# Performance work log

Hardware: AMD Instinct MI355X
Metric: run time of the kernel (lower is better)

## Reference

```python
import jax, jax.numpy as jnp
import numpy as np

N_NODES = 100000
LN_EPS = 1e-5


def setup_inputs() -> dict:
    key = jax.random.key(0)
    ks = jax.random.split(key, 5)
    d = 128
    E = 1600000
    x = jax.random.normal(ks[0], (N_NODES, d), dtype=jnp.float32)
    edge_index = jax.random.randint(ks[1], (2, E), 0, N_NODES, dtype=jnp.int64)
    # PyG Linear default init ~ kaiming-uniform-ish; simple scaled normal is fine for a reference
    W_l = jax.random.normal(ks[2], (d, d), dtype=jnp.float32) / jnp.sqrt(d).astype(jnp.float32)
    b_l = jnp.zeros((d,), dtype=jnp.float32)
    W_r = jax.random.normal(ks[3], (d, d), dtype=jnp.float32) / jnp.sqrt(d).astype(jnp.float32)
    ln_gamma = jnp.ones((d,), dtype=jnp.float32)
    ln_beta = jnp.zeros((d,), dtype=jnp.float32)
    return {"x": x, "edge_index": edge_index, "W_l": W_l, "b_l": b_l,
            "W_r": W_r, "ln_gamma": ln_gamma, "ln_beta": ln_beta}


def _sage_block(x, edge_index, W_l, b_l, W_r, ln_gamma, ln_beta):
    src, dst = edge_index[0], edge_index[1]
    # gather source features along edges, scatter-mean into destination nodes
    msg = x[src]                                            # [E, d]
    agg = jax.ops.segment_sum(msg, dst, num_segments=N_NODES)  # [N, d]
    cnt = jax.ops.segment_sum(jnp.ones_like(dst, dtype=x.dtype), dst,
                              num_segments=N_NODES)
    agg = agg / jnp.maximum(cnt, 1.0)[:, None]              # mean aggregation
    # SAGEConv: lin_l(agg) + lin_r(x); lin_l has bias, lin_r does not
    f = agg @ W_l.T + b_l + x @ W_r.T                        # [N, d]
    # GELU (exact erf form, matching torch F.gelu default)
    f = jax.nn.gelu(f, approximate=False)
    # LayerNorm over feature dim
    mu = jnp.mean(f, axis=-1, keepdims=True)
    var = jnp.var(f, axis=-1, keepdims=True)
    f = (f - mu) * jax.lax.rsqrt(var + LN_EPS) * ln_gamma + ln_beta
    # dropout is identity in eval mode; residual
    return f + x


def reference(x, edge_index, W_l, b_l, W_r, ln_gamma, ln_beta):
    return _sage_block(x, edge_index, W_l, b_l, W_r, ln_gamma, ln_beta)
```

## Files before the change

### kernel.cpp

```cpp
#include <hip/hip_runtime.h>
#include <math.h>

#define D 128
#define LN_EPS 1e-5f
#define CAP 48
#define BINW 512
#define BIN_CAP 12288
#define PA_EDGES 8192

typedef unsigned int uint;
typedef unsigned short ushort;
typedef __attribute__((ext_vector_type(8))) short short8;
typedef __attribute__((ext_vector_type(4))) float floatx4;

__device__ __forceinline__ floatx4 mfma16(short8 a, short8 b, floatx4 c) {
    return __builtin_amdgcn_mfma_f32_16x16x32_bf16(a, b, c, 0, 0, 0);
}

__device__ __forceinline__ ushort f2bf(float f) {
    uint u = __float_as_uint(f);
    u += 0x7FFFu + ((u >> 16) & 1u);
    return (ushort)(u >> 16);
}

__device__ __forceinline__ float fast_exp2(float x) {
#if __has_builtin(__builtin_amdgcn_exp2f)
    return __builtin_amdgcn_exp2f(x);
#else
    return exp2f(x);
#endif
}
__device__ __forceinline__ float fast_rcp(float x) {
#if __has_builtin(__builtin_amdgcn_rcpf)
    return __builtin_amdgcn_rcpf(x);
#else
    return 1.f / x;
#endif
}

__device__ __forceinline__ float gelu_f(float x) {
    float z = x + 0.044715f * x * x * x;
    float e = fast_exp2(fminf(2.3022082f * z, 80.f));
    return x * e * fast_rcp(e + 1.f);
}

__global__ __launch_bounds__(256) void setup_kernel(
        const float* __restrict__ x,
        const float* __restrict__ Wl, const float* __restrict__ Wr,
        ushort* __restrict__ xh, ushort* __restrict__ Wswhi,
        int* __restrict__ cursor, int* __restrict__ bin_cnt, int nbc4,
        int n_nodes, int rn) {
    const int tid = threadIdx.x;
    const int cb = blockIdx.x;
    const int g = cb & 7, cid = cb >> 3;
    const int lrow = cid * 16 + (tid >> 4);
    const int row = g * rn + lrow;
    if (row < n_nodes && lrow < rn) {
        const int base = row * D + (tid & 15) * 8;
        float4 a = *(const float4*)&x[base];
        float4 b = *(const float4*)&x[base + 4];
        union { ushort h[8]; uint4 v; } pk;
        pk.h[0] = f2bf(a.x); pk.h[1] = f2bf(a.y); pk.h[2] = f2bf(a.z); pk.h[3] = f2bf(a.w);
        pk.h[4] = f2bf(b.x); pk.h[5] = f2bf(b.y); pk.h[6] = f2bf(b.z); pk.h[7] = f2bf(b.w);
        *(uint4*)&xh[base] = pk.v;
    }
    const int t = cb * 256 + tid;
    if (t < 16)
        *(uint4*)&xh[(size_t)n_nodes * D + t * 8] = make_uint4(0u, 0u, 0u, 0u);
    if (t * 4 < n_nodes)
        *(int4*)&cursor[t * 4] = make_int4(0, 0, 0, 0);
    if (t < nbc4)
        *(int4*)&bin_cnt[t * 4] = make_int4(0, 0, 0, 0);
    if (t < 8 * 8 * 64) {
        int tt = t >> 9;
        int rem = t & 511;
        int s  = rem >> 6;
        int lane = rem & 63;
        int lc = lane & 15, lq = lane >> 4;
        int col = tt * 16 + lc;
        int k0  = s * 32 + lq * 8;
        union { ushort h[8]; uint4 v; } hi;
        #pragma unroll
        for (int j = 0; j < 8; j++) {
            int k = k0 + j;
            float w = (k < 128) ? Wl[col * 128 + k] : Wr[col * 128 + (k - 128)];
            hi.h[j] = f2bf(w);
        }
        *(uint4*)&Wswhi[t * 8] = hi.v;
    }
}

__global__ void transpose_w(const float* __restrict__ Wl, const float* __restrict__ Wr,
                            float* __restrict__ WlT, float* __restrict__ WrT) {
    int t = blockIdx.x * blockDim.x + threadIdx.x;
    if (t < D * D) {
        int j = t & (D - 1);
        int k = t >> 7;
        WlT[k * D + j] = Wl[j * D + k];
        WrT[k * D + j] = Wr[j * D + k];
    }
}

__global__ __launch_bounds__(256) void bin_edges(
        const int* __restrict__ src, const int* __restrict__ dst,
        int* __restrict__ bin_cnt, int2* __restrict__ bins,
        int E, int nb) {
    __shared__ int hist[256];
    __shared__ int base[256];
    const int tid = threadIdx.x;
    const int e0 = blockIdx.x * PA_EDGES;
    for (int i = tid; i < nb; i += 256) hist[i] = 0;
    __syncthreads();
    #pragma unroll 4
    for (int k = 0; k < PA_EDGES / 256; k++) {
        int e = e0 + k * 256 + tid;
        if (e < E) atomicAdd(&hist[dst[e] >> 9], 1);
    }
    __syncthreads();
    for (int i = tid; i < nb; i += 256) {
        int c = hist[i];
        base[i] = c ? atomicAdd(&bin_cnt[i * 16], c) : 0;
        hist[i] = 0;
    }
    __syncthreads();
    #pragma unroll 4
    for (int k = 0; k < PA_EDGES / 256; k++) {
        int e = e0 + k * 256 + tid;
        if (e < E) {
            int d = dst[e];
            int b = d >> 9;
            int pos = base[b] + atomicAdd(&hist[b], 1);
            if (pos < BIN_CAP)
                bins[(size_t)b * BIN_CAP + pos] = make_int2(src[e], d);
        }
    }
}

__global__ __launch_bounds__(256) void fill_from_bins(
        const int2* __restrict__ bins, const int* __restrict__ bin_cnt,
        int* __restrict__ cursor, int* __restrict__ bucket, int n_nodes) {
    __shared__ int lcur[BINW];
    const int tid = threadIdx.x;
    const int b = blockIdx.x;
    const int d0 = b << 9;
    for (int i = tid; i < BINW; i += 256) lcur[i] = 0;
    __syncthreads();
    int cnt = bin_cnt[b * 16];
    if (cnt > BIN_CAP) cnt = BIN_CAP;
    const int2* __restrict__ bp = bins + (size_t)b * BIN_CAP;
    for (int i = tid; i < cnt; i += 256) {
        int2 e = bp[i];
        int pos = atomicAdd(&lcur[e.y - d0], 1);
        if (pos < CAP) bucket[(size_t)e.y * CAP + pos] = e.x;
    }
    __syncthreads();
    for (int i = tid; i < BINW; i += 256) {
        int d = d0 + i;
        if (d < n_nodes) cursor[d] = lcur[i];
    }
}

__global__ __launch_bounds__(256) void fill_cap(
        const int* __restrict__ src, const int* __restrict__ dst,
        int* __restrict__ cursor, int* __restrict__ bucket, int E, int rn) {
    const int g   = blockIdx.x & 7;
    const int cid = blockIdx.x >> 3;
    const int lo = g * rn, hi = lo + rn;
    for (int e = cid * 256 + threadIdx.x; e < E; e += 65536) {
        int d = dst[e];
        if (d >= lo && d < hi) {
            int pos = atomicAdd(&cursor[d], 1);
            if (pos < CAP) bucket[(size_t)d * CAP + pos] = src[e];
        }
    }
}

__global__ __launch_bounds__(256) void agg_cap(
        const uint4* __restrict__ xu4,
        const int* __restrict__ cursor, const int* __restrict__ bucket,
        uint4* __restrict__ aggu4, int n_nodes, int rn, int zrow) {
    const int wave = threadIdx.x >> 6, lane = threadIdx.x & 63;
    const int grp = blockIdx.x & 7;
    const int cid = blockIdx.x >> 3;
    const int g = lane >> 4;
    const int sub = lane & 15;
    const int ln = cid * 8 + wave * 2;
    const int nodeA = grp * rn + ln;
    if (ln >= rn || nodeA >= n_nodes) return;
    const bool hasB = (ln + 1 < rn) && (nodeA + 1 < n_nodes);
    const int nodeB = hasB ? nodeA + 1 : nodeA;
    const int degA = cursor[nodeA];
    const int degB = cursor[nodeB];
    const int mA = degA < CAP ? degA : CAP;
    const int mB = hasB ? (degB < CAP ? degB : CAP) : 0;
    const int* __restrict__ rowA = bucket + (size_t)nodeA * CAP;
    const int* __restrict__ rowB = bucket + (size_t)nodeB * CAP;
    const int mMax = mA > mB ? mA : mB;

    float sA[8] = {0.f, 0.f, 0.f, 0.f, 0.f, 0.f, 0.f, 0.f};
    float sB[8] = {0.f, 0.f, 0.f, 0.f, 0.f, 0.f, 0.f, 0.f};

    #define ACC(s, v)                                          \
        { s[0] += __uint_as_float((v).x << 16);                \
          s[1] += __uint_as_float((v).x & 0xFFFF0000u);        \
          s[2] += __uint_as_float((v).y << 16);                \
          s[3] += __uint_as_float((v).y & 0xFFFF0000u);        \
          s[4] += __uint_as_float((v).z << 16);                \
          s[5] += __uint_as_float((v).z & 0xFFFF0000u);        \
          s[6] += __uint_as_float((v).w << 16);                \
          s[7] += __uint_as_float((v).w & 0xFFFF0000u); }

    for (int e = 0; e < mMax; e += 16) {
        if (e < mA) {
            int a0 = (e + g      < mA) ? rowA[e + g]      : zrow;
            int a1 = (e + 4 + g  < mA) ? rowA[e + 4 + g]  : zrow;
            int a2 = (e + 8 + g  < mA) ? rowA[e + 8 + g]  : zrow;
            int a3 = (e + 12 + g < mA) ? rowA[e + 12 + g] : zrow;
            uint4 va = xu4[(size_t)a0 * 16 + sub];
            uint4 vb = xu4[(size_t)a1 * 16 + sub];
            uint4 vc = xu4[(size_t)a2 * 16 + sub];
            uint4 vd = xu4[(size_t)a3 * 16 + sub];
            ACC(sA, va) ACC(sA, vb) ACC(sA, vc) ACC(sA, vd)
        }
        if (e < mB) {
            int b0 = (e + g      < mB) ? rowB[e + g]      : zrow;
            int b1 = (e + 4 + g  < mB) ? rowB[e + 4 + g]  : zrow;
            int b2 = (e + 8 + g  < mB) ? rowB[e + 8 + g]  : zrow;
            int b3 = (e + 12 + g < mB) ? rowB[e + 12 + g] : zrow;
            uint4 va = xu4[(size_t)b0 * 16 + sub];
            uint4 vb = xu4[(size_t)b1 * 16 + sub];
            uint4 vc = xu4[(size_t)b2 * 16 + sub];
            uint4 vd = xu4[(size_t)b3 * 16 + sub];
            ACC(sB, va) ACC(sB, vb) ACC(sB, vc) ACC(sB, vd)
        }
    }
    #undef ACC

    #pragma unroll
    for (int mm = 16; mm <= 32; mm <<= 1)
        #pragma unroll
        for (int j = 0; j < 8; j++) {
            sA[j] += __shfl_xor(sA[j], mm);
            sB[j] += __shfl_xor(sB[j], mm);
        }

    if (g == 0) {
        float inv = 1.f / (float)(degA > 0 ? degA : 1);
        uint4 o;
        o.x = (uint)f2bf(sA[0] * inv) | (((uint)f2bf(sA[1] * inv)) << 16);
        o.y = (uint)f2bf(sA[2] * inv) | (((uint)f2bf(sA[3] * inv)) << 16);
        o.z = (uint)f2bf(sA[4] * inv) | (((uint)f2bf(sA[5] * inv)) << 16);
        o.w = (uint)f2bf(sA[6] * inv) | (((uint)f2bf(sA[7] * inv)) << 16);
        aggu4[(size_t)nodeA * 16 + sub] = o;
    } else if (g == 1 && hasB) {
        float inv = 1.f / (float)(degB > 0 ? degB : 1);
        uint4 o;
        o.x = (uint)f2bf(sB[0] * inv) | (((uint)f2bf(sB[1] * inv)) << 16);
        o.y = (uint)f2bf(sB[2] * inv) | (((uint)f2bf(sB[3] * inv)) << 16);
        o.z = (uint)f2bf(sB[4] * inv) | (((uint)f2bf(sB[5] * inv)) << 16);
        o.w = (uint)f2bf(sB[6] * inv) | (((uint)f2bf(sB[7] * inv)) << 16);
        aggu4[(size_t)nodeB * 16 + sub] = o;
    }
}

__global__ __launch_bounds__(256) void dense_kernel(
        const ushort* __restrict__ aggh, const ushort* __restrict__ xh,
        const ushort* __restrict__ Wswhi,
        const float* __restrict__ bl, const float* __restrict__ gam,
        const float* __restrict__ bet,
        float* __restrict__ out, int n_nodes, int rn) {
    const int tid = threadIdx.x, wave = tid >> 6, lane = tid & 63;
    const int lc = lane & 15, lq = lane >> 4;
    const int g = blockIdx.x & 7, cid = blockIdx.x >> 3;
    const int m0 = g * rn + cid * 64 + wave * 16;

    int arow = m0 + lc;
    if (arow >= n_nodes) arow = n_nodes - 1;
    const int ko = lq * 8;

    short8 av[8];
    #pragma unroll
    for (int s = 0; s < 8; s++) {
        const ushort* ap = (s < 4)
            ? (aggh + (size_t)arow * D + s * 32 + ko)
            : (xh   + (size_t)arow * D + (s - 4) * 32 + ko);
        av[s] = *(const short8*)ap;
    }

    floatx4 acc[8];
    #pragma unroll
    for (int t = 0; t < 8; t++) acc[t] = (floatx4){0.f, 0.f, 0.f, 0.f};

    #pragma unroll
    for (int s = 0; s < 8; s++) {
        #pragma unroll
        for (int t = 0; t < 8; t++) {
            short8 bh = *(const short8*)&Wswhi[((t * 8 + s) * 64 + lane) * 8];
            acc[t] = mfma16(av[s], bh, acc[t]);
        }
    }

    float psum[4] = {0.f, 0.f, 0.f, 0.f};
    float psq[4]  = {0.f, 0.f, 0.f, 0.f};
    #pragma unroll
    for (int t = 0; t < 8; t++) {
        float bb = bl[t * 16 + lc];
        #pragma unroll
        for (int r = 0; r < 4; r++) {
            float f = acc[t][r] + bb;
            float gg = gelu_f(f);
            acc[t][r] = gg;
            psum[r] += gg;
            psq[r]  += gg * gg;
        }
    }
    #pragma unroll
    for (int m = 8; m >= 1; m >>= 1) {
        #pragma unroll
        for (int r = 0; r < 4; r++) {
            psum[r] += __shfl_xor(psum[r], m);
            psq[r]  += __shfl_xor(psq[r], m);
        }
    }
    float mu[4], rsq[4];
    #pragma unroll
    for (int r = 0; r < 4; r++) {
        mu[r] = psum[r] * (1.f / (float)D);
        float var = psq[r] * (1.f / (float)D) - mu[r] * mu[r];
        rsq[r] = rsqrtf(var + LN_EPS);
    }
    #pragma unroll
    for (int t = 0; t < 8; t++) {
        int col = t * 16 + lc;
        float gm = gam[col], bt = bet[col];
        #pragma unroll
        for (int r = 0; r < 4; r++) {
            int row = m0 + lq * 4 + r;
            if (row < n_nodes) {
                float xr = __uint_as_float(((uint)xh[(size_t)row * D + col]) << 16);
                out[(size_t)row * D + col] = (acc[t][r] - mu[r]) * rsq[r] * gm + bt + xr;
            }
        }
    }
}

#define NBF 32
#define LSTR 132
__global__ __launch_bounds__(256, 4) void fused_cap(
        const float* __restrict__ x,
        const float* __restrict__ WlT, const float* __restrict__ WrT,
        const float* __restrict__ bl,  const float* __restrict__ gam,
        const float* __restrict__ bet,
        const int* __restrict__ cursor, const int* __restrict__ bucket,
        float* __restrict__ out, int n_nodes) {
    __shared__ __align__(16) float sagg[NBF * LSTR];
    __shared__ __align__(16) float sx[NBF * LSTR];
    const int tid   = threadIdx.x;
    const int node0 = blockIdx.x * NBF;
    const int hl = tid & 31, hw = tid >> 5, hl4 = hl * 4;
    #pragma unroll
    for (int r = 0; r < NBF / 8; r++) {
        const int n = r * 8 + hw;
        const int g = node0 + n;
        float s0 = 0.f, s1 = 0.f, s2 = 0.f, s3 = 0.f;
        float4 xv = make_float4(0.f, 0.f, 0.f, 0.f);
        float inv = 0.f;
        if (g < n_nodes) {
            const int deg = cursor[g];
            const int m = deg < CAP ? deg : CAP;
            const int* row = bucket + (size_t)g * CAP;
            int e = 0;
            for (; e + 4 <= m; e += 4) {
                int i0 = row[e], i1 = row[e + 1], i2 = row[e + 2], i3 = row[e + 3];
                float4 a0 = *(const float4*)&x[i0 * D + hl4];
                float4 a1 = *(const float4*)&x[i1 * D + hl4];
                float4 a2 = *(const float4*)&x[i2 * D + hl4];
                float4 a3 = *(const float4*)&x[i3 * D + hl4];
                s0 += (a0.x + a1.x) + (a2.x + a3.x);
                s1 += (a0.y + a1.y) + (a2.y + a3.y);
                s2 += (a0.z + a1.z) + (a2.z + a3.z);
                s3 += (a0.w + a1.w) + (a2.w + a3.w);
            }
            for (; e < m; e++) {
                float4 a = *(const float4*)&x[row[e] * D + hl4];
                s0 += a.x; s1 += a.y; s2 += a.z; s3 += a.w;
            }
            inv = 1.f / (float)(deg > 0 ? deg : 1);
            xv = *(const float4*)&x[g * D + hl4];
        }
        *(float4*)&sagg[n * LSTR + hl4] = make_float4(s0 * inv, s1 * inv, s2 * inv, s3 * inv);
        *(float4*)&sx[n * LSTR + hl4]   = xv;
    }
    __syncthreads();
    const int tj = tid & 31, tn = tid >> 5;
    const int j0 = tj * 4, n0 = tn * 4;
    float4 blv = *(const float4*)&bl[j0];
    float acc[4][4];
    #pragma unroll
    for (int nn = 0; nn < 4; nn++) {
        acc[0][nn] = blv.x; acc[1][nn] = blv.y; acc[2][nn] = blv.z; acc[3][nn] = blv.w;
    }
    for (int kc = 0; kc < D; kc += 4) {
        float4 av[4], bv[4];
        #pragma unroll
        for (int nn = 0; nn < 4; nn++) {
            av[nn] = *(const float4*)&sagg[(n0 + nn) * LSTR + kc];
            bv[nn] = *(const float4*)&sx[(n0 + nn) * LSTR + kc];
        }
        #pragma unroll
        for (int kk = 0; kk < 4; kk++) {
            float4 wl = *(const float4*)&WlT[(kc + kk) * D + j0];
            float4 wr = *(const float4*)&WrT[(kc + kk) * D + j0];
            float wlv[4] = {wl.x, wl.y, wl.z, wl.w};
            float wrv[4] = {wr.x, wr.y, wr.z, wr.w};
            #pragma unroll
            for (int nn = 0; nn < 4; nn++) {
                float a = ((const float*)&av[nn])[kk];
                float b = ((const float*)&bv[nn])[kk];
                #pragma unroll
                for (int jj = 0; jj < 4; jj++)
                    acc[jj][nn] = fmaf(wlv[jj], a, fmaf(wrv[jj], b, acc[jj][nn]));
            }
        }
    }
    float psum[4] = {0.f, 0.f, 0.f, 0.f};
    float psq[4]  = {0.f, 0.f, 0.f, 0.f};
    #pragma unroll
    for (int jj = 0; jj < 4; jj++)
        #pragma unroll
        for (int nn = 0; nn < 4; nn++) {
            float f = acc[jj][nn];
            float g = 0.5f * f * (1.f + erff(f * 0.70710678118654752440f));
            acc[jj][nn] = g;
            psum[nn] += g;
            psq[nn]  += g * g;
        }
    #pragma unroll
    for (int m = 16; m >= 1; m >>= 1) {
        #pragma unroll
        for (int nn = 0; nn < 4; nn++) {
            psum[nn] += __shfl_xor(psum[nn], m);
            psq[nn]  += __shfl_xor(psq[nn], m);
        }
    }
    float4 gv = *(const float4*)&gam[j0];
    float4 bv4 = *(const float4*)&bet[j0];
    float gvv[4] = {gv.x, gv.y, gv.z, gv.w};
    float bvv[4] = {bv4.x, bv4.y, bv4.z, bv4.w};
    #pragma unroll
    for (int nn = 0; nn < 4; nn++) {
        int node = node0 + n0 + nn;
        if (node < n_nodes) {
            float m2  = psum[nn] * (1.f / (float)D);
            float var = psq[nn] * (1.f / (float)D) - m2 * m2;
            float rs  = rsqrtf(var + LN_EPS);
            float4 xr = *(const float4*)&x[node * D + j0];
            float xrv[4] = {xr.x, xr.y, xr.z, xr.w};
            float o[4];
            #pragma unroll
            for (int jj = 0; jj < 4; jj++)
                o[jj] = (acc[jj][nn] - m2) * rs * gvv[jj] + bvv[jj] + xrv[jj];
            *(float4*)&out[node * D + j0] = make_float4(o[0], o[1], o[2], o[3]);
        }
    }
}

static inline size_t align_up(size_t v, size_t a) { return (v + a - 1) & ~(a - 1); }

extern "C" void kernel_launch(void* const* d_in, const int* in_sizes, int n_in,
                              void* d_out, int out_size, void* d_ws, size_t ws_size,
                              hipStream_t stream) {
    const float* x   = (const float*)d_in[0];
    const int*   ei  = (const int*)d_in[1];
    const float* Wl  = (const float*)d_in[2];
    const float* bl  = (const float*)d_in[3];
    const float* Wr  = (const float*)d_in[4];
    const float* gam = (const float*)d_in[5];
    const float* bet = (const float*)d_in[6];
    float* out = (float*)d_out;

    const int N = in_sizes[0] / D;
    const int E = in_sizes[1] / 2;
    const int* src = ei;
    const int* dst = ei + E;
    const int rn = (((N + 7) / 8) + 63) & ~63;
    const int NB = (N + BINW - 1) >> 9;

    int* bucket = (int*)d_out;
    int2* bins = (int2*)(bucket + (size_t)N * CAP);

    char* p = (char*)d_ws;
    int* cursor = (int*)p;
    p = (char*)align_up((size_t)(cursor + N), 256);
    int* bin_cnt = (int*)p;
    p = (char*)align_up((size_t)(bin_cnt + (size_t)NB * 16), 256);
    ushort* Wswhi = (ushort*)p;
    float* WlT = (float*)Wswhi;
    float* WrT = WlT + D * D;
    p = (char*)align_up((size_t)p + 2 * D * D * sizeof(float), 256);
    ushort* xh   = (ushort*)p;
    ushort* aggh = xh + (size_t)(N + 8) * D;
    size_t need_full = (size_t)((char*)(aggh + (size_t)N * D) - (char*)d_ws);

    size_t out_bytes_needed = (size_t)N * CAP * sizeof(int)
                            + (size_t)NB * BIN_CAP * sizeof(int2);
    const int nbc4 = NB * 4;
    const int blocksA = (E + PA_EDGES - 1) / PA_EDGES;

    if (ws_size >= need_full && NB <= 256 &&
        (size_t)out_size * sizeof(float) >= out_bytes_needed) {
        setup_kernel<<<8 * ((rn + 15) / 16), 256, 0, stream>>>(
            x, Wl, Wr, xh, Wswhi, cursor, bin_cnt, nbc4, N, rn);
        bin_edges<<<blocksA, 256, 0, stream>>>(src, dst, bin_cnt, bins, E, NB);
        fill_from_bins<<<NB, 256, 0, stream>>>(bins, bin_cnt, cursor, bucket, N);
        agg_cap<<<8 * ((rn + 7) / 8), 256, 0, stream>>>(
            (const uint4*)xh, cursor, bucket, (uint4*)aggh, N, rn, N);
        dense_kernel<<<8 * (rn / 64), 256, 0, stream>>>(
            aggh, xh, Wswhi, bl, gam, bet, out, N, rn);
    } else if (ws_size >= need_full &&
               (size_t)out_size * sizeof(float) >= (size_t)N * CAP * sizeof(int)) {
        setup_kernel<<<8 * ((rn + 15) / 16), 256, 0, stream>>>(
            x, Wl, Wr, xh, Wswhi, cursor, bin_cnt, 0, N, rn);
        fill_cap<<<2048, 256, 0, stream>>>(src, dst, cursor, bucket, E, rn);
        agg_cap<<<8 * ((rn + 7) / 8), 256, 0, stream>>>(
            (const uint4*)xh, cursor, bucket, (uint4*)aggh, N, rn, N);
        dense_kernel<<<8 * (rn / 64), 256, 0, stream>>>(
            aggh, xh, Wswhi, bl, gam, bet, out, N, rn);
    } else {
        (void)hipMemsetAsync(cursor, 0, (size_t)N * sizeof(int), stream);
        transpose_w<<<(D * D + 255) / 256, 256, 0, stream>>>(Wl, Wr, WlT, WrT);
        fill_cap<<<2048, 256, 0, stream>>>(src, dst, cursor, bucket, E, rn);
        fused_cap<<<(N + NBF - 1) / NBF, 256, 0, stream>>>(
            x, WlT, WrT, bl, gam, bet, cursor, bucket, out, N);
    }
}
```

Before: 265.7 us.

## Fuse neighbor aggregation into dense MFMA kernel and pack bin entries

Merges the aggregation and dense kernels into one. Each block aggregates its 64 nodes into a shared-memory bf16 tile, which the MFMA stage then reads, so the aggregated features are never written to and reread from global memory. Bin entries are also packed from int2 into a single uint (23-bit source index plus 9-bit local destination), halving binning traffic. The bucket moves into the workspace, and the fused kernel has fewer blocks, each running a serial 16-node aggregation loop per wave, which may reduce the parallelism available to hide gather latency.

```diff
diff --git a/kernel.cpp b/kernel.cpp
--- a/kernel.cpp
+++ b/kernel.cpp
@@ -7,6 +7,7 @@
 #define BINW 512
 #define BIN_CAP 12288
 #define PA_EDGES 8192
+#define LSTR2 136
 
 typedef unsigned int uint;
 typedef unsigned short ushort;
@@ -103,7 +104,7 @@
 
 __global__ __launch_bounds__(256) void bin_edges(
         const int* __restrict__ src, const int* __restrict__ dst,
-        int* __restrict__ bin_cnt, int2* __restrict__ bins,
+        int* __restrict__ bin_cnt, uint* __restrict__ bins,
         int E, int nb) {
     __shared__ int hist[256];
     __shared__ int base[256];
@@ -131,13 +132,14 @@
             int b = d >> 9;
             int pos = base[b] + atomicAdd(&hist[b], 1);
             if (pos < BIN_CAP)
-                bins[(size_t)b * BIN_CAP + pos] = make_int2(src[e], d);
+                bins[(size_t)b * BIN_CAP + pos] =
+                    (uint)src[e] | (((uint)d & 511u) << 23);
         }
     }
 }
 
 __global__ __launch_bounds__(256) void fill_from_bins(
-        const int2* __restrict__ bins, const int* __restrict__ bin_cnt,
+        const uint* __restrict__ bins, const int* __restrict__ bin_cnt,
         int* __restrict__ cursor, int* __restrict__ bucket, int n_nodes) {
     __shared__ int lcur[BINW];
     const int tid = threadIdx.x;
@@ -147,11 +149,12 @@
     __syncthreads();
     int cnt = bin_cnt[b * 16];
     if (cnt > BIN_CAP) cnt = BIN_CAP;
-    const int2* __restrict__ bp = bins + (size_t)b * BIN_CAP;
+    const uint* __restrict__ bp = bins + (size_t)b * BIN_CAP;
     for (int i = tid; i < cnt; i += 256) {
-        int2 e = bp[i];
-        int pos = atomicAdd(&lcur[e.y - d0], 1);
-        if (pos < CAP) bucket[(size_t)e.y * CAP + pos] = e.x;
+        uint v = bp[i];
+        int di = (int)(v >> 23);
+        int pos = atomicAdd(&lcur[di], 1);
+        if (pos < CAP) bucket[(size_t)(d0 + di) * CAP + pos] = (int)(v & 0x7FFFFFu);
     }
     __syncthreads();
     for (int i = tid; i < BINW; i += 256) {
@@ -175,30 +178,20 @@
     }
 }
 
-__global__ __launch_bounds__(256) void agg_cap(
+__global__ __launch_bounds__(256) void agg_dense(
         const uint4* __restrict__ xu4,
         const int* __restrict__ cursor, const int* __restrict__ bucket,
-        uint4* __restrict__ aggu4, int n_nodes, int rn, int zrow) {
-    const int wave = threadIdx.x >> 6, lane = threadIdx.x & 63;
-    const int grp = blockIdx.x & 7;
-    const int cid = blockIdx.x >> 3;
-    const int g = lane >> 4;
+        const ushort* __restrict__ xh, const ushort* __restrict__ Wswhi,
+        const float* __restrict__ bl, const float* __restrict__ gam,
+        const float* __restrict__ bet,
+        float* __restrict__ out, int n_nodes, int rn, int zrow) {
+    __shared__ __align__(16) ushort sagg[64 * LSTR2];
+    const int tid = threadIdx.x, wave = tid >> 6, lane = tid & 63;
+    const int g = blockIdx.x & 7, cid = blockIdx.x >> 3;
+    const int m0 = g * rn + cid * 64 + wave * 16;
+
+    const int eg = lane >> 4;
     const int sub = lane & 15;
-    const int ln = cid * 8 + wave * 2;
-    const int nodeA = grp * rn + ln;
-    if (ln >= rn || nodeA >= n_nodes) return;
-    const bool hasB = (ln + 1 < rn) && (nodeA + 1 < n_nodes);
-    const int nodeB = hasB ? nodeA + 1 : nodeA;
-    const int degA = cursor[nodeA];
-    const int degB = cursor[nodeB];
-    const int mA = degA < CAP ? degA : CAP;
-    const int mB = hasB ? (degB < CAP ? degB : CAP) : 0;
-    const int* __restrict__ rowA = bucket + (size_t)nodeA * CAP;
-    const int* __restrict__ rowB = bucket + (size_t)nodeB * CAP;
-    const int mMax = mA > mB ? mA : mB;
-
-    float sA[8] = {0.f, 0.f, 0.f, 0.f, 0.f, 0.f, 0.f, 0.f};
-    float sB[8] = {0.f, 0.f, 0.f, 0.f, 0.f, 0.f, 0.f, 0.f};
 
     #define ACC(s, v)                                          \
         { s[0] += __uint_as_float((v).x << 16);                \
@@ -210,70 +203,76 @@
           s[6] += __uint_as_float((v).w << 16);                \
           s[7] += __uint_as_float((v).w & 0xFFFF0000u); }
 
-    for (int e = 0; e < mMax; e += 16) {
-        if (e < mA) {
-            int a0 = (e + g      < mA) ? rowA[e + g]      : zrow;
-            int a1 = (e + 4 + g  < mA) ? rowA[e + 4 + g]  : zrow;
-            int a2 = (e + 8 + g  < mA) ? rowA[e + 8 + g]  : zrow;
-            int a3 = (e + 12 + g < mA) ? rowA[e + 12 + g] : zrow;
-            uint4 va = xu4[(size_t)a0 * 16 + sub];
-            uint4 vb = xu4[(size_t)a1 * 16 + sub];
-            uint4 vc = xu4[(size_t)a2 * 16 + sub];
-            uint4 vd = xu4[(size_t)a3 * 16 + sub];
-            ACC(sA, va) ACC(sA, vb) ACC(sA, vc) ACC(sA, vd)
-        }
-        if (e < mB) {
-            int b0 = (e + g      < mB) ? rowB[e + g]      : zrow;
-            int b1 = (e + 4 + g  < mB) ? rowB[e + 4 + g]  : zrow;
-            int b2 = (e + 8 + g  < mB) ? rowB[e + 8 + g]  : zrow;
-            int b3 = (e + 12 + g < mB) ? rowB[e + 12 + g] : zrow;
-            uint4 va = xu4[(size_t)b0 * 16 + sub];
-            uint4 vb = xu4[(size_t)b1 * 16 + sub];
-            uint4 vc = xu4[(size_t)b2 * 16 + sub];
-            uint4 vd = xu4[(size_t)b3 * 16 + sub];
-            ACC(sB, va) ACC(sB, vb) ACC(sB, vc) ACC(sB, vd)
+    for (int np = 0; np < 16; np += 2) {
+        const int nodeA = m0 + np;
+        const bool okA = nodeA < n_nodes;
+        const bool okB = nodeA + 1 < n_nodes;
+        const int degA = okA ? cursor[nodeA] : 0;
+        const int degB = okB ? cursor[nodeA + 1] : 0;
+        const int mA = degA < CAP ? degA : CAP;
+        const int mB = degB < CAP ? degB : CAP;
+        const int* __restrict__ rowA = bucket + (size_t)nodeA * CAP;
+        const int* __restrict__ rowB = rowA + CAP;
+        const int mMax = mA > mB ? mA : mB;
+
+        float sA[8] = {0.f, 0.f, 0.f, 0.f, 0.f, 0.f, 0.f, 0.f};
+        float sB[8] = {0.f, 0.f, 0.f, 0.f, 0.f, 0.f, 0.f, 0.f};
+
+        for (int e = 0; e < mMax; e += 16) {
+            if (e < mA) {
+                int a0 = (e + eg      < mA) ? rowA[e + eg]      : zrow;
+                int a1 = (e + 4 + eg  < mA) ? rowA[e + 4 + eg]  : zrow;
+                int a2 = (e + 8 + eg  < mA) ? rowA[e + 8 + eg]  : zrow;
+                int a3 = (e + 12 + eg < mA) ? rowA[e + 12 + eg] : zrow;
+                uint4 va = xu4[(size_t)a0 * 16 + sub];
+                uint4 vb = xu4[(size_t)a1 * 16 + sub];
+                uint4 vc = xu4[(size_t)a2 * 16 + sub];
+                uint4 vd = xu4[(size_t)a3 * 16 + sub];
+                ACC(sA, va) ACC(sA, vb) ACC(sA, vc) ACC(sA, vd)
+            }
+            if (e < mB) {
+                int b0 = (e + eg      < mB) ? rowB[e + eg]      : zrow;
+                int b1 = (e + 4 + eg  < mB) ? rowB[e + 4 + eg]  : zrow;
+                int b2 = (e + 8 + eg  < mB) ? rowB[e + 8 + eg]  : zrow;
+                int b3 = (e + 12 + eg < mB) ? rowB[e + 12 + eg] : zrow;
+                uint4 va = xu4[(size_t)b0 * 16 + sub];
+                uint4 vb = xu4[(size_t)b1 * 16 + sub];
+                uint4 vc = xu4[(size_t)b2 * 16 + sub];
+                uint4 vd = xu4[(size_t)b3 * 16 + sub];
+                ACC(sB, va) ACC(sB, vb) ACC(sB, vc) ACC(sB, vd)
+            }
+        }
+
+        #pragma unroll
+        for (int mm = 16; mm <= 32; mm <<= 1)
+            #pragma unroll
+            for (int j = 0; j < 8; j++) {
+                sA[j] += __shfl_xor(sA[j], mm);
+                sB[j] += __shfl_xor(sB[j], mm);
+            }
+
+        if (eg == 0) {
+            float inv = 1.f / (float)(degA > 0 ? degA : 1);
+            uint4 o;
+            o.x = (uint)f2bf(sA[0] * inv) | (((uint)f2bf(sA[1] * inv)) << 16);
+            o.y = (uint)f2bf(sA[2] * inv) | (((uint)f2bf(sA[3] * inv)) << 16);
+            o.z = (uint)f2bf(sA[4] * inv) | (((uint)f2bf(sA[5] * inv)) << 16);
+            o.w = (uint)f2bf(sA[6] * inv) | (((uint)f2bf(sA[7] * inv)) << 16);
+            *(uint4*)&sagg[(wave * 16 + np) * LSTR2 + sub * 8] = o;
+        } else if (eg == 1) {
+            float inv = 1.f / (float)(degB > 0 ? degB : 1);
+            uint4 o;
+            o.x = (uint)f2bf(sB[0] * inv) | (((uint)f2bf(sB[1] * inv)) << 16);
+            o.y = (uint)f2bf(sB[2] * inv) | (((uint)f2bf(sB[3] * inv)) << 16);
+            o.z = (uint)f2bf(sB[4] * inv) | (((uint)f2bf(sB[5] * inv)) << 16);
+            o.w = (uint)f2bf(sB[6] * inv) | (((uint)f2bf(sB[7] * inv)) << 16);
+            *(uint4*)&sagg[(wave * 16 + np + 1) * LSTR2 + sub * 8] = o;
         }
     }
     #undef ACC
-
-    #pragma unroll
-    for (int mm = 16; mm <= 32; mm <<= 1)
-        #pragma unroll
-        for (int j = 0; j < 8; j++) {
-            sA[j] += __shfl_xor(sA[j], mm);
-            sB[j] += __shfl_xor(sB[j], mm);
-        }
-
-    if (g == 0) {
-        float inv = 1.f / (float)(degA > 0 ? degA : 1);
-        uint4 o;
-        o.x = (uint)f2bf(sA[0] * inv) | (((uint)f2bf(sA[1] * inv)) << 16);
-        o.y = (uint)f2bf(sA[2] * inv) | (((uint)f2bf(sA[3] * inv)) << 16);
-        o.z = (uint)f2bf(sA[4] * inv) | (((uint)f2bf(sA[5] * inv)) << 16);
-        o.w = (uint)f2bf(sA[6] * inv) | (((uint)f2bf(sA[7] * inv)) << 16);
-        aggu4[(size_t)nodeA * 16 + sub] = o;
-    } else if (g == 1 && hasB) {
-        float inv = 1.f / (float)(degB > 0 ? degB : 1);
-        uint4 o;
-        o.x = (uint)f2bf(sB[0] * inv) | (((uint)f2bf(sB[1] * inv)) << 16);
-        o.y = (uint)f2bf(sB[2] * inv) | (((uint)f2bf(sB[3] * inv)) << 16);
-        o.z = (uint)f2bf(sB[4] * inv) | (((uint)f2bf(sB[5] * inv)) << 16);
-        o.w = (uint)f2bf(sB[6] * inv) | (((uint)f2bf(sB[7] * inv)) << 16);
-        aggu4[(size_t)nodeB * 16 + sub] = o;
-    }
-}
-
-__global__ __launch_bounds__(256) void dense_kernel(
-        const ushort* __restrict__ aggh, const ushort* __restrict__ xh,
-        const ushort* __restrict__ Wswhi,
-        const float* __restrict__ bl, const float* __restrict__ gam,
-        const float* __restrict__ bet,
-        float* __restrict__ out, int n_nodes, int rn) {
-    const int tid = threadIdx.x, wave = tid >> 6, lane = tid & 63;
+    __syncthreads();
+
     const int lc = lane & 15, lq = lane >> 4;
-    const int g = blockIdx.x & 7, cid = blockIdx.x >> 3;
-    const int m0 = g * rn + cid * 64 + wave * 16;
-
     int arow = m0 + lc;
     if (arow >= n_nodes) arow = n_nodes - 1;
     const int ko = lq * 8;
@@ -281,10 +280,10 @@
     short8 av[8];
     #pragma unroll
     for (int s = 0; s < 8; s++) {
-        const ushort* ap = (s < 4)
-            ? (aggh + (size_t)arow * D + s * 32 + ko)
-            : (xh   + (size_t)arow * D + (s - 4) * 32 + ko);
-        av[s] = *(const short8*)ap;
+        if (s < 4)
+            av[s] = *(const short8*)&sagg[(wave * 16 + lc) * LSTR2 + s * 32 + ko];
+        else
+            av[s] = *(const short8*)&xh[(size_t)arow * D + (s - 4) * 32 + ko];
     }
 
     floatx4 acc[8];
@@ -486,11 +485,12 @@
     const int rn = (((N + 7) / 8) + 63) & ~63;
     const int NB = (N + BINW - 1) >> 9;
 
-    int* bucket = (int*)d_out;
-    int2* bins = (int2*)(bucket + (size_t)N * CAP);
+    int* cursor;
+    int* bucket;
+    uint* bins = (uint*)d_out;
 
     char* p = (char*)d_ws;
-    int* cursor = (int*)p;
+    cursor = (int*)p;
     p = (char*)align_up((size_t)(cursor + N), 256);
     int* bin_cnt = (int*)p;
     p = (char*)align_up((size_t)(bin_cnt + (size_t)NB * 16), 256);
@@ -499,38 +499,34 @@
     float* WrT = WlT + D * D;
     p = (char*)align_up((size_t)p + 2 * D * D * sizeof(float), 256);
     ushort* xh   = (ushort*)p;
-    ushort* aggh = xh + (size_t)(N + 8) * D;
-    size_t need_full = (size_t)((char*)(aggh + (size_t)N * D) - (char*)d_ws);
-
-    size_t out_bytes_needed = (size_t)N * CAP * sizeof(int)
-                            + (size_t)NB * BIN_CAP * sizeof(int2);
+    p = (char*)align_up((size_t)(xh + (size_t)(N + 8) * D), 256);
+    bucket = (int*)p;
+    size_t need_full = (size_t)((char*)(bucket + (size_t)N * CAP) - (char*)d_ws);
+
+    size_t out_bytes_needed = (size_t)NB * BIN_CAP * sizeof(uint);
     const int nbc4 = NB * 4;
     const int blocksA = (E + PA_EDGES - 1) / PA_EDGES;
 
-    if (ws_size >= need_full && NB <= 256 &&
+    if (ws_size >= need_full && NB <= 256 && N <= (1 << 23) &&
         (size_t)out_size * sizeof(float) >= out_bytes_needed) {
         setup_kernel<<<8 * ((rn + 15) / 16), 256, 0, stream>>>(
             x, Wl, Wr, xh, Wswhi, cursor, bin_cnt, nbc4, N, rn);
         bin_edges<<<blocksA, 256, 0, stream>>>(src, dst, bin_cnt, bins, E, NB);
         fill_from_bins<<<NB, 256, 0, stream>>>(bins, bin_cnt, cursor, bucket, N);
-        agg_cap<<<8 * ((rn + 7) / 8), 256, 0, stream>>>(
-            (const uint4*)xh, cursor, bucket, (uint4*)aggh, N, rn, N);
-        dense_kernel<<<8 * (rn / 64), 256, 0, stream>>>(
-            aggh, xh, Wswhi, bl, gam, bet, out, N, rn);
-    } else if (ws_size >= need_full &&
-               (size_t)out_size * sizeof(float) >= (size_t)N * CAP * sizeof(int)) {
+        agg_dense<<<8 * (rn / 64), 256, 0, stream>>>(
+            (const uint4*)xh, cursor, bucket, xh, Wswhi, bl, gam, bet, out, N, rn, N);
+    } else if (ws_size >= need_full) {
         setup_kernel<<<8 * ((rn + 15) / 16), 256, 0, stream>>>(
-            x, Wl, Wr, xh, Wswhi, cursor, bin_cnt, 0, N, rn);
+            x, Wl, Wr, xh, Wswhi, cursor, bin_cnt, NB <= 256 ? nbc4 : 0, N, rn);
         fill_cap<<<2048, 256, 0, stream>>>(src, dst, cursor, bucket, E, rn);
-        agg_cap<<<8 * ((rn + 7) / 8), 256, 0, stream>>>(
-            (const uint4*)xh, cursor, bucket, (uint4*)aggh, N, rn, N);
-        dense_kernel<<<8 * (rn / 64), 256, 0, stream>>>(
-            aggh, xh, Wswhi, bl, gam, bet, out, N, rn);
+        agg_dense<<<8 * (rn / 64), 256, 0, stream>>>(
+            (const uint4*)xh, cursor, bucket, xh, Wswhi, bl, gam, bet, out, N, rn, N);
     } else {
+        int* bucket_o = (int*)d_out;
         (void)hipMemsetAsync(cursor, 0, (size_t)N * sizeof(int), stream);
         transpose_w<<<(D * D + 255) / 256, 256, 0, stream>>>(Wl, Wr, WlT, WrT);
-        fill_cap<<<2048, 256, 0, stream>>>(src, dst, cursor, bucket, E, rn);
+        fill_cap<<<2048, 256, 0, stream>>>(src, dst, cursor, bucket_o, E, rn);
         fused_cap<<<(N + NBF - 1) / NBF, 256, 0, stream>>>(
-            x, WlT, WrT, bl, gam, bet, cursor, bucket, out, N);
-    }
-}
+            x, WlT, WrT, bl, gam, bet, cursor, bucket_o, out, N);
+    }
+}
```

After: 295.2 us. 1.11x slower.
